# Kernel tuning notes

Hardware: AMD Instinct MI355X
Metric: run time of the kernel (lower is better)

Reference implementation:

```python
import jax, jax.numpy as jnp
import numpy as np

EMB = 768
HEADS = 8

def setup_inputs() -> dict:
    key = jax.random.key(0)
    ks = jax.random.split(key, 5)
    x = jax.random.normal(ks[0], (8, 2048, EMB), dtype=jnp.float32)
    s = 1.0 / np.sqrt(EMB)
    W_qkv = jax.random.normal(ks[1], (EMB, 3 * EMB), dtype=jnp.float32) * s
    b_qkv = jnp.zeros((3 * EMB,), dtype=jnp.float32)
    W_proj = jax.random.normal(ks[2], (EMB, EMB), dtype=jnp.float32) * s
    b_proj = jnp.zeros((EMB,), dtype=jnp.float32)
    return {"x": x, "W_qkv": W_qkv, "b_qkv": b_qkv, "W_proj": W_proj, "b_proj": b_proj}

def reference(x, W_qkv, b_qkv, W_proj, b_proj):
    B, N, E = x.shape
    H = HEADS
    D = E // H
    qkv = x @ W_qkv + b_qkv  # [B, N, 3E]
    q, k, v = jnp.split(qkv, 3, axis=-1)
    # [B, N, E] -> [B, H, N, D]
    def heads(t):
        return t.reshape(B, N, H, D).transpose(0, 2, 1, 3)
    q, k, v = heads(q), heads(k), heads(v)
    # NOTE: original scales by 1/sqrt(emb_size), not 1/sqrt(head_dim)
    dots = jnp.einsum('bhnd,bhmd->bhnm', q, k) / jnp.sqrt(jnp.float32(E))
    attn = jax.nn.softmax(dots, axis=-1)  # dropout inactive (eval mode)
    out = jnp.einsum('bhnm,bhmd->bhnd', attn, v)
    out = out.transpose(0, 2, 1, 3).reshape(B, N, E)
    return out @ W_proj + b_proj
```

## Files before the change

### kernel.cpp

```cpp
#include <hip/hip_runtime.h>
#include <hip/hip_bf16.h>

typedef __attribute__((ext_vector_type(8))) short bf16x8;
typedef __attribute__((ext_vector_type(4))) short bf16x4;
typedef __attribute__((ext_vector_type(4))) float f32x4;
typedef __attribute__((ext_vector_type(16))) float f32x16;
typedef __attribute__((ext_vector_type(4))) unsigned int uint4v;

__device__ __forceinline__ short f2bf(float f) {
    unsigned int u = __float_as_uint(f);
    u += 0x7FFFu + ((u >> 16) & 1u);
    return (short)(u >> 16);
}

__device__ __forceinline__ unsigned cvtpk(float lo, float hi) {
    unsigned r;
    asm("v_cvt_pk_bf16_f32 %0, %1, %2" : "=v"(r) : "v"(lo), "v"(hi));
    return r;
}

__device__ __forceinline__ void gload_lds16(const void* g, void* l) {
    __builtin_amdgcn_global_load_lds(
        (const __attribute__((address_space(1))) void*)g,
        (__attribute__((address_space(3))) void*)l, 16, 0, 0);
}

__global__ __launch_bounds__(256) void prep_kernel(
    const float* __restrict__ x, short* __restrict__ xb,
    const float* __restrict__ Wqkv, short* __restrict__ WqkvT,
    const float* __restrict__ Wproj, short* __restrict__ WprojT)
{
    __shared__ float tile[64][65];
    const int t = threadIdx.x;
    const unsigned bx = blockIdx.x;
    if (bx < 2048) {
        size_t base = (size_t)bx * 256 + t;
#pragma unroll
        for (int it = 0; it < 6; ++it) {
            size_t i = base + (size_t)it * 524288;
            const f32x4 v = *(const f32x4*)(x + i * 4);
            bf16x4 o;
            o[0] = f2bf(v[0]); o[1] = f2bf(v[1]); o[2] = f2bf(v[2]); o[3] = f2bf(v[3]);
            *(bf16x4*)(xb + i * 4) = o;
        }
        return;
    }
    const float* W; short* WT; int C, tiles_x, tt;
    if (bx < 2480) { W = Wqkv;  WT = WqkvT;  C = 2304; tiles_x = 36; tt = (int)bx - 2048; }
    else           { W = Wproj; WT = WprojT; C = 768;  tiles_x = 12; tt = (int)bx - 2480; }
    const int R = 768;
    const int bc = (tt % tiles_x) * 64;
    const int br = (tt / tiles_x) * 64;
#pragma unroll
    for (int i = 0; i < 16; ++i) {
        int o = t + 256 * i;
        int r = o >> 6, c = o & 63;
        tile[r][c] = W[(size_t)(br + r) * C + bc + c];
    }
    __syncthreads();
#pragma unroll
    for (int i = 0; i < 16; ++i) {
        int o = t + 256 * i;
        int c = o >> 6, r = o & 63;
        WT[(size_t)(bc + c) * R + br + r] = f2bf(tile[r][c]);
    }
}

__global__ __launch_bounds__(256, 4) void gemm1_kernel(
    const short* __restrict__ A, const short* __restrict__ BT,
    const float* __restrict__ bias,
    short* __restrict__ Qh, short* __restrict__ Kh, short* __restrict__ Vt)
{
    __shared__ short As[128][64];
    __shared__ short Bs[128][64];
    const int K = 768;
    const int t = threadIdx.x;
    const int w = t >> 6, l = t & 63;
    const int wr = w >> 1, wc = w & 1;
    const int lr = l & 15, lg = l >> 4;

    const int srow = w * 32 + (l >> 3);
    const int scol = (l & 7) * 8;
    const short* Ag = A + (size_t)blockIdx.x * 128 * K + (size_t)srow * K + scol;
    const short* Bg = BT + (size_t)blockIdx.y * 128 * K + (size_t)srow * K + scol;

    const f32x4 z4 = {0.f, 0.f, 0.f, 0.f};
    f32x4 acc[4][4];
#pragma unroll
    for (int i = 0; i < 4; ++i)
#pragma unroll
        for (int j = 0; j < 4; ++j) acc[i][j] = z4;

    for (int kt = 0; kt < K; kt += 64) {
#pragma unroll
        for (int i = 0; i < 4; ++i) {
            gload_lds16(Ag + kt + (size_t)(i * 8) * K, &As[w * 32 + i * 8][0]);
            gload_lds16(Bg + kt + (size_t)(i * 8) * K, &Bs[w * 32 + i * 8][0]);
        }
        __syncthreads();
#pragma unroll
        for (int kk = 0; kk < 2; ++kk) {
            bf16x8 af[4], bfr[4];
#pragma unroll
            for (int mi = 0; mi < 4; ++mi)
                af[mi] = *(const bf16x8*)&As[wr * 64 + mi * 16 + lr][kk * 32 + lg * 8];
#pragma unroll
            for (int ni = 0; ni < 4; ++ni)
                bfr[ni] = *(const bf16x8*)&Bs[wc * 64 + ni * 16 + lr][kk * 32 + lg * 8];
#pragma unroll
            for (int mi = 0; mi < 4; ++mi)
#pragma unroll
                for (int ni = 0; ni < 4; ++ni)
                    acc[mi][ni] = __builtin_amdgcn_mfma_f32_16x16x32_bf16(
                        af[mi], bfr[ni], acc[mi][ni], 0, 0, 0);
        }
        __syncthreads();
    }

    const float qs = 0.05205877f;
    const int rb = blockIdx.x * 128 + wr * 64;
    const int cb = blockIdx.y * 128 + wc * 64;
#pragma unroll
    for (int ni = 0; ni < 4; ++ni) {
        const int c = cb + ni * 16 + lr;
        const float bv = bias[c];
        const int which = (c >= 1536) ? 2 : (c >= 768 ? 1 : 0);
        const int cc = c - which * 768;
        const int h = cc / 96;
        const int d = cc - h * 96;
#pragma unroll
        for (int mi = 0; mi < 4; ++mi) {
            const int r0 = rb + mi * 16 + lg * 4;
            const int b = r0 >> 11, n0 = r0 & 2047;
            const int hb = b * 8 + h;
            if (which == 2) {
                bf16x4 pk;
#pragma unroll
                for (int r = 0; r < 4; ++r) pk[r] = f2bf(acc[mi][ni][r] + bv);
                *(bf16x4*)&Vt[((size_t)hb * 96 + d) * 2048 + n0] = pk;
            } else if (which == 1) {
#pragma unroll
                for (int r = 0; r < 4; ++r)
                    Kh[((size_t)hb * 2048 + n0 + r) * 96 + d] = f2bf(acc[mi][ni][r] + bv);
            } else {
#pragma unroll
                for (int r = 0; r < 4; ++r)
                    Qh[((size_t)hb * 2048 + n0 + r) * 96 + d] = f2bf((acc[mi][ni][r] + bv) * qs);
            }
        }
    }
}

__global__ __launch_bounds__(256, 2) void attn_kernel(
    const short* __restrict__ Qh, const short* __restrict__ Kh,
    const short* __restrict__ Vt, short* __restrict__ AO)
{
    __shared__ __align__(16) char smem[54272];
    short (*Ks0)[104] = (short (*)[104])smem;
    short (*Ks1)[104] = (short (*)[104])(smem + 13312);
    short (*Vs0)[72]  = (short (*)[72])(smem + 26624);
    short (*Vs1)[72]  = (short (*)[72])(smem + 40448);
    short (*Qs)[104]  = (short (*)[104])smem;
    float (*ltab)[32] = (float (*)[32])smem;

    const int t = threadIdx.x;
    const int w = t >> 6, l = t & 63;
    const int ql = l & 31, hi = l >> 5;

    const unsigned L = blockIdx.y * 16 + blockIdx.x;
    const int bh = (int)((L & 7) + 8 * (L >> 7));
    const int qt = (int)((L >> 3) & 15);

    const short* Qg = Qh + (size_t)bh * 2048 * 96 + (size_t)qt * 128 * 96;
    const short* Kg = Kh + (size_t)bh * 2048 * 96;
    const short* Vg = Vt + (size_t)bh * 96 * 2048;

    bf16x8 kreg[3], vreg[3];
#pragma unroll
    for (int i = 0; i < 3; ++i) {
        int o = t + 256 * i;
        kreg[i] = *(const bf16x8*)(Kg + 8 * (size_t)o);
        vreg[i] = *(const bf16x8*)(Vg + (size_t)(o >> 3) * 2048 + (o & 7) * 8);
    }

#pragma unroll
    for (int i = 0; i < 6; ++i) {
        int o = t + 256 * i;
        *(bf16x8*)&Qs[o / 12][(o % 12) * 8] = *(const bf16x8*)(Qg + 8 * (size_t)o);
    }
    __syncthreads();
    bf16x8 qf[6];
#pragma unroll
    for (int kk = 0; kk < 6; ++kk)
        qf[kk] = *(const bf16x8*)&Qs[w * 32 + ql][kk * 16 + hi * 8];
    __syncthreads();

#pragma unroll
    for (int i = 0; i < 3; ++i) {
        int o = t + 256 * i;
        *(bf16x8*)&Ks0[o / 12][(o % 12) * 8] = kreg[i];
        *(bf16x8*)&Vs0[o >> 3][(o & 7) * 8] = vreg[i];
    }
#pragma unroll
    for (int i = 0; i < 3; ++i) {
        int o = t + 256 * i;
        kreg[i] = *(const bf16x8*)(Kg + (size_t)64 * 96 + 8 * (size_t)o);
        vreg[i] = *(const bf16x8*)(Vg + (size_t)(o >> 3) * 2048 + 64 + (o & 7) * 8);
    }
    __syncthreads();

    f32x16 oacc[3];
#pragma unroll
    for (int i = 0; i < 3; ++i)
#pragma unroll
        for (int r = 0; r < 16; ++r) oacc[i][r] = 0.f;
    float lacc = 0.f;

    auto iter = [&](int kt, short (*rK)[104], short (*rV)[72],
                    short (*wK)[104], short (*wV)[72]) {
        if (kt < 31) {
#pragma unroll
            for (int i = 0; i < 3; ++i) {
                int o = t + 256 * i;
                *(bf16x8*)&wK[o / 12][(o % 12) * 8] = kreg[i];
                *(bf16x8*)&wV[o >> 3][(o & 7) * 8] = vreg[i];
            }
        }
        if (kt < 30) {
            const size_t koff = (size_t)(kt + 2) * 64 * 96;
            const int moff = (kt + 2) * 64;
#pragma unroll
            for (int i = 0; i < 3; ++i) {
                int o = t + 256 * i;
                kreg[i] = *(const bf16x8*)(Kg + koff + 8 * (size_t)o);
                vreg[i] = *(const bf16x8*)(Vg + (size_t)(o >> 3) * 2048 + moff + (o & 7) * 8);
            }
        }

        f32x16 sa0, sa1;
#pragma unroll
        for (int r = 0; r < 16; ++r) { sa0[r] = 0.f; sa1[r] = 0.f; }
        __builtin_amdgcn_s_setprio(1);
#pragma unroll
        for (int kk = 0; kk < 6; ++kk) {
            bf16x8 kf0 = *(const bf16x8*)&rK[ql][kk * 16 + hi * 8];
            bf16x8 kf1 = *(const bf16x8*)&rK[32 + ql][kk * 16 + hi * 8];
            sa0 = __builtin_amdgcn_mfma_f32_32x32x16_bf16(kf0, qf[kk], sa0, 0, 0, 0);
            sa1 = __builtin_amdgcn_mfma_f32_32x32x16_bf16(kf1, qf[kk], sa1, 0, 0, 0);
        }
        __builtin_amdgcn_s_setprio(0);

        bf16x8 pa[4];
#pragma unroll
        for (int mi = 0; mi < 2; ++mi) {
            float p[16];
#pragma unroll
            for (int r = 0; r < 16; ++r) {
                p[r] = __builtin_amdgcn_exp2f(mi == 0 ? sa0[r] : sa1[r]);
                lacc += p[r];
            }
            unsigned x0 = cvtpk(p[0], p[1]),  y0 = cvtpk(p[4], p[5]);
            unsigned x1 = cvtpk(p[2], p[3]),  y1 = cvtpk(p[6], p[7]);
            unsigned x2 = cvtpk(p[8], p[9]),  y2 = cvtpk(p[12], p[13]);
            unsigned x3 = cvtpk(p[10], p[11]), y3 = cvtpk(p[14], p[15]);
            asm("v_permlane32_swap_b32 %0, %1" : "+v"(x0), "+v"(y0));
            asm("v_permlane32_swap_b32 %0, %1" : "+v"(x1), "+v"(y1));
            asm("v_permlane32_swap_b32 %0, %1" : "+v"(x2), "+v"(y2));
            asm("v_permlane32_swap_b32 %0, %1" : "+v"(x3), "+v"(y3));
            uint4v uA; uA[0] = x0; uA[1] = x1; uA[2] = y0; uA[3] = y1;
            uint4v uB; uB[0] = x2; uB[1] = x3; uB[2] = y2; uB[3] = y3;
            pa[mi * 2 + 0] = __builtin_bit_cast(bf16x8, uA);
            pa[mi * 2 + 1] = __builtin_bit_cast(bf16x8, uB);
        }

        __builtin_amdgcn_s_setprio(1);
#pragma unroll
        for (int kb = 0; kb < 4; ++kb) {
#pragma unroll
            for (int db = 0; db < 3; ++db) {
                bf16x8 vf = *(const bf16x8*)&rV[db * 32 + ql][kb * 16 + hi * 8];
                oacc[db] = __builtin_amdgcn_mfma_f32_32x32x16_bf16(pa[kb], vf, oacc[db], 0, 0, 0);
            }
        }
        __builtin_amdgcn_s_setprio(0);
        __syncthreads();
    };

    for (int kt = 0; kt < 32; kt += 2) {
        iter(kt,     Ks0, Vs0, Ks1, Vs1);
        iter(kt + 1, Ks1, Vs1, Ks0, Vs0);
    }

    float lsum = lacc + __shfl_xor(lacc, 32);
    if (l < 32) ltab[w][l] = lsum;
    asm volatile("s_waitcnt lgkmcnt(0)" ::: "memory");

    float linv[16];
#pragma unroll
    for (int r = 0; r < 16; ++r) {
        const int q = (r & 3) + 8 * (r >> 2) + 4 * hi;
        linv[r] = 1.0f / ltab[w][q];
    }

    const int b = bh >> 3, h = bh & 7;
    const size_t rowbase = (size_t)b * 2048 + qt * 128 + w * 32;
#pragma unroll
    for (int db = 0; db < 3; ++db) {
#pragma unroll
        for (int r = 0; r < 16; ++r) {
            const int q = (r & 3) + 8 * (r >> 2) + 4 * hi;
            AO[(rowbase + q) * 768 + h * 96 + db * 32 + ql] = f2bf(oacc[db][r] * linv[r]);
        }
    }
}

__global__ __launch_bounds__(256, 4) void gemm2_kernel(
    const short* __restrict__ A, const short* __restrict__ BT,
    const float* __restrict__ bias, float* __restrict__ out)
{
    __shared__ short As[128][64];
    __shared__ short Bs[128][64];
    const int K = 768;
    const int t = threadIdx.x;
    const int w = t >> 6, l = t & 63;
    const int wr = w >> 1, wc = w & 1;
    const int lr = l & 15, lg = l >> 4;

    const int srow = w * 32 + (l >> 3);
    const int scol = (l & 7) * 8;
    const short* Ag = A + (size_t)blockIdx.x * 128 * K + (size_t)srow * K + scol;
    const short* Bg = BT + (size_t)blockIdx.y * 128 * K + (size_t)srow * K + scol;

    const f32x4 z4 = {0.f, 0.f, 0.f, 0.f};
    f32x4 acc[4][4];
#pragma unroll
    for (int i = 0; i < 4; ++i)
#pragma unroll
        for (int j = 0; j < 4; ++j) acc[i][j] = z4;

    for (int kt = 0; kt < K; kt += 64) {
#pragma unroll
        for (int i = 0; i < 4; ++i) {
            gload_lds16(Ag + kt + (size_t)(i * 8) * K, &As[w * 32 + i * 8][0]);
            gload_lds16(Bg + kt + (size_t)(i * 8) * K, &Bs[w * 32 + i * 8][0]);
        }
        __syncthreads();
#pragma unroll
        for (int kk = 0; kk < 2; ++kk) {
            bf16x8 af[4], bfr[4];
#pragma unroll
            for (int mi = 0; mi < 4; ++mi)
                af[mi] = *(const bf16x8*)&As[wr * 64 + mi * 16 + lr][kk * 32 + lg * 8];
#pragma unroll
            for (int ni = 0; ni < 4; ++ni)
                bfr[ni] = *(const bf16x8*)&Bs[wc * 64 + ni * 16 + lr][kk * 32 + lg * 8];
#pragma unroll
            for (int mi = 0; mi < 4; ++mi)
#pragma unroll
                for (int ni = 0; ni < 4; ++ni)
                    acc[mi][ni] = __builtin_amdgcn_mfma_f32_16x16x32_bf16(
                        af[mi], bfr[ni], acc[mi][ni], 0, 0, 0);
        }
        __syncthreads();
    }

    const int rb = blockIdx.x * 128 + wr * 64;
    const int cb = blockIdx.y * 128 + wc * 64;
#pragma unroll
    for (int ni = 0; ni < 4; ++ni) {
        const int c = cb + ni * 16 + lr;
        const float bv = bias[c];
#pragma unroll
        for (int mi = 0; mi < 4; ++mi) {
            const int r0 = rb + mi * 16 + lg * 4;
#pragma unroll
            for (int r = 0; r < 4; ++r)
                out[(size_t)(r0 + r) * 768 + c] = acc[mi][ni][r] + bv;
        }
    }
}

extern "C" void kernel_launch(void* const* d_in, const int* in_sizes, int n_in,
                              void* d_out, int out_size, void* d_ws, size_t ws_size,
                              hipStream_t stream) {
    const float* x     = (const float*)d_in[0];
    const float* Wqkv  = (const float*)d_in[1];
    const float* bqkv  = (const float*)d_in[2];
    const float* Wproj = (const float*)d_in[3];
    const float* bproj = (const float*)d_in[4];
    float* out = (float*)d_out;

    char* ws = (char*)d_ws;
    short* xb     = (short*)(ws);
    short* WqkvT  = (short*)(ws + 25165824);
    short* WprojT = (short*)(ws + 28704768);
    short* Qh     = (short*)(ws + 29884416);
    short* Kh     = (short*)(ws + 55050240);
    short* Vt     = (short*)(ws + 80216064);
    short* AO     = xb;

    prep_kernel<<<2624, 256, 0, stream>>>(x, xb, Wqkv, WqkvT, Wproj, WprojT);
    gemm1_kernel<<<dim3(128, 18), 256, 0, stream>>>(xb, WqkvT, bqkv, Qh, Kh, Vt);
    attn_kernel<<<dim3(16, 64), 256, 0, stream>>>(Qh, Kh, Vt, AO);
    gemm2_kernel<<<dim3(128, 6), 256, 0, stream>>>(AO, WprojT, bproj, out);
}
```

Before: 236.1 us.

## Fuse fp32-to-bf16 conversion of x into the QKV GEMM load path

Removes the separate pass that converts x to bf16 in the prep kernel. The QKV GEMM now stages fp32 x tiles in LDS and converts them to bf16 with packed conversion instructions as it builds MFMA fragments. This saves a full write and re-read of a bf16 copy of x. In exchange, the GEMM loads twice as many A bytes, once per column block (18 times), uses a larger LDS footprint, and drops its occupancy hint from 4 to 3.

```diff
diff --git a/kernel.cpp b/kernel.cpp
--- a/kernel.cpp
+++ b/kernel.cpp
@@ -26,28 +26,15 @@
 }
 
 __global__ __launch_bounds__(256) void prep_kernel(
-    const float* __restrict__ x, short* __restrict__ xb,
     const float* __restrict__ Wqkv, short* __restrict__ WqkvT,
     const float* __restrict__ Wproj, short* __restrict__ WprojT)
 {
     __shared__ float tile[64][65];
     const int t = threadIdx.x;
     const unsigned bx = blockIdx.x;
-    if (bx < 2048) {
-        size_t base = (size_t)bx * 256 + t;
-#pragma unroll
-        for (int it = 0; it < 6; ++it) {
-            size_t i = base + (size_t)it * 524288;
-            const f32x4 v = *(const f32x4*)(x + i * 4);
-            bf16x4 o;
-            o[0] = f2bf(v[0]); o[1] = f2bf(v[1]); o[2] = f2bf(v[2]); o[3] = f2bf(v[3]);
-            *(bf16x4*)(xb + i * 4) = o;
-        }
-        return;
-    }
     const float* W; short* WT; int C, tiles_x, tt;
-    if (bx < 2480) { W = Wqkv;  WT = WqkvT;  C = 2304; tiles_x = 36; tt = (int)bx - 2048; }
-    else           { W = Wproj; WT = WprojT; C = 768;  tiles_x = 12; tt = (int)bx - 2480; }
+    if (bx < 432) { W = Wqkv;  WT = WqkvT;  C = 2304; tiles_x = 36; tt = (int)bx; }
+    else          { W = Wproj; WT = WprojT; C = 768;  tiles_x = 12; tt = (int)bx - 432; }
     const int R = 768;
     const int bc = (tt % tiles_x) * 64;
     const int br = (tt / tiles_x) * 64;
@@ -66,12 +53,12 @@
     }
 }
 
-__global__ __launch_bounds__(256, 4) void gemm1_kernel(
-    const short* __restrict__ A, const short* __restrict__ BT,
+__global__ __launch_bounds__(256, 3) void gemm1_kernel(
+    const float* __restrict__ X, const short* __restrict__ BT,
     const float* __restrict__ bias,
     short* __restrict__ Qh, short* __restrict__ Kh, short* __restrict__ Vt)
 {
-    __shared__ short As[128][64];
+    __shared__ float Asf[128][64];
     __shared__ short Bs[128][64];
     const int K = 768;
     const int t = threadIdx.x;
@@ -79,10 +66,8 @@
     const int wr = w >> 1, wc = w & 1;
     const int lr = l & 15, lg = l >> 4;
 
-    const int srow = w * 32 + (l >> 3);
-    const int scol = (l & 7) * 8;
-    const short* Ag = A + (size_t)blockIdx.x * 128 * K + (size_t)srow * K + scol;
-    const short* Bg = BT + (size_t)blockIdx.y * 128 * K + (size_t)srow * K + scol;
+    const float* Ag = X + (size_t)(blockIdx.x * 128 + w * 32 + (l >> 4)) * K + (l & 15) * 4;
+    const short* Bg = BT + (size_t)blockIdx.y * 128 * K + (size_t)(w * 32 + (l >> 3)) * K + (l & 7) * 8;
 
     const f32x4 z4 = {0.f, 0.f, 0.f, 0.f};
     f32x4 acc[4][4];
@@ -93,17 +78,26 @@
 
     for (int kt = 0; kt < K; kt += 64) {
 #pragma unroll
-        for (int i = 0; i < 4; ++i) {
-            gload_lds16(Ag + kt + (size_t)(i * 8) * K, &As[w * 32 + i * 8][0]);
+        for (int i = 0; i < 8; ++i)
+            gload_lds16(Ag + kt + (size_t)(i * 4) * K, &Asf[w * 32 + i * 4][0]);
+#pragma unroll
+        for (int i = 0; i < 4; ++i)
             gload_lds16(Bg + kt + (size_t)(i * 8) * K, &Bs[w * 32 + i * 8][0]);
-        }
         __syncthreads();
 #pragma unroll
         for (int kk = 0; kk < 2; ++kk) {
             bf16x8 af[4], bfr[4];
 #pragma unroll
-            for (int mi = 0; mi < 4; ++mi)
-                af[mi] = *(const bf16x8*)&As[wr * 64 + mi * 16 + lr][kk * 32 + lg * 8];
+            for (int mi = 0; mi < 4; ++mi) {
+                const f32x4* Ap = (const f32x4*)&Asf[wr * 64 + mi * 16 + lr][kk * 32 + lg * 8];
+                const f32x4 a0 = Ap[0], a1 = Ap[1];
+                uint4v u;
+                u[0] = cvtpk(a0[0], a0[1]);
+                u[1] = cvtpk(a0[2], a0[3]);
+                u[2] = cvtpk(a1[0], a1[1]);
+                u[3] = cvtpk(a1[2], a1[3]);
+                af[mi] = __builtin_bit_cast(bf16x8, u);
+            }
 #pragma unroll
             for (int ni = 0; ni < 4; ++ni)
                 bfr[ni] = *(const bf16x8*)&Bs[wc * 64 + ni * 16 + lr][kk * 32 + lg * 8];
@@ -391,16 +385,15 @@
     float* out = (float*)d_out;
 
     char* ws = (char*)d_ws;
-    short* xb     = (short*)(ws);
+    short* AO     = (short*)(ws);
     short* WqkvT  = (short*)(ws + 25165824);
     short* WprojT = (short*)(ws + 28704768);
     short* Qh     = (short*)(ws + 29884416);
     short* Kh     = (short*)(ws + 55050240);
     short* Vt     = (short*)(ws + 80216064);
-    short* AO     = xb;
-
-    prep_kernel<<<2624, 256, 0, stream>>>(x, xb, Wqkv, WqkvT, Wproj, WprojT);
-    gemm1_kernel<<<dim3(128, 18), 256, 0, stream>>>(xb, WqkvT, bqkv, Qh, Kh, Vt);
+
+    prep_kernel<<<576, 256, 0, stream>>>(Wqkv, WqkvT, Wproj, WprojT);
+    gemm1_kernel<<<dim3(128, 18), 256, 0, stream>>>(x, WqkvT, bqkv, Qh, Kh, Vt);
     attn_kernel<<<dim3(16, 64), 256, 0, stream>>>(Qh, Kh, Vt, AO);
     gemm2_kernel<<<dim3(128, 6), 256, 0, stream>>>(AO, WprojT, bproj, out);
 }
```

Measured after the change: 290.2 us. 22.9% more time.
